# Optimization experiments

Measured on AMD Instinct MI355X. Metric: run time of the kernel, lower is better.

## Reference

```python
import jax, jax.numpy as jnp
import numpy as np

NUM_GRAPHS = 256  # B: number of graphs in the ragged batch
EMBED = 256       # input_dim / MHA embed_dim
N_NODES = 200000


def setup_inputs() -> dict:
    key = jax.random.key(0)
    k1, k2, k3, k4, k5, k6 = jax.random.split(key, 6)
    x = jax.random.normal(k1, (N_NODES, EMBED), dtype=jnp.float32)
    in_proj_w = jax.random.normal(k2, (3 * EMBED, EMBED), dtype=jnp.float32) * 0.02
    in_proj_b = jax.random.normal(k3, (3 * EMBED,), dtype=jnp.float32) * 0.02
    out_proj_w = jax.random.normal(k4, (EMBED, EMBED), dtype=jnp.float32) * 0.02
    out_proj_b = jax.random.normal(k5, (EMBED,), dtype=jnp.float32) * 0.02
    batch = jnp.sort(jax.random.randint(k6, (N_NODES,), 0, NUM_GRAPHS)).astype(jnp.int64)
    return {"x": x, "in_proj_w": in_proj_w, "in_proj_b": in_proj_b,
            "out_proj_w": out_proj_w, "out_proj_b": out_proj_b, "batch": batch}


def reference(x, in_proj_w, in_proj_b, out_proj_w, out_proj_b, batch):
    E = x.shape[1]
    # global_mean_pool: per-graph mean of node features -> [B, E]
    sums = jax.ops.segment_sum(x, batch, num_segments=NUM_GRAPHS)
    counts = jax.ops.segment_sum(jnp.ones((x.shape[0],), x.dtype), batch,
                                 num_segments=NUM_GRAPHS)
    g = sums / jnp.maximum(counts, 1.0)[:, None]  # [B, E]
    # MultiheadAttention with a single K/V vector per graph: softmax over S=1
    # is identically 1, so attention output = out_proj(V_proj(g)) for every
    # query node of that graph (Q path contributes nothing).
    Wv = in_proj_w[2 * E:3 * E]
    bv = in_proj_b[2 * E:3 * E]
    v = g @ Wv.T + bv                       # [B, E] value projection
    out_graph = v @ out_proj_w.T + out_proj_b  # [B, E] output projection
    # broadcast back to nodes (torch.cat over per-graph slices)
    return out_graph[batch]                 # [N, E]
```

## Files before the change

### kernel.cpp

```cpp
#include <hip/hip_runtime.h>

#define EMBED   256
#define NGRAPH  256
#define P       4
#define BLOCK1  512
#define NW1     (BLOCK1 / 64)
#define WPG     (P * NW1)
#define BLOCK3  256
#define NB3     2048

typedef float f32x4 __attribute__((ext_vector_type(4)));

__global__ __launch_bounds__(BLOCK1, 8) void seg_partial(
    const float* __restrict__ x, const int* __restrict__ batch,
    float* __restrict__ partial, int nNodes) {
  const int g  = blockIdx.x >> 2;
  const int p  = blockIdx.x & (P - 1);
  const int t  = threadIdx.x;
  const int q  = t >> 6;
  const int c4 = t & 63;

  int n0, n1;
  { int a = 0, b = nNodes;
    while (a < b) { int m = (a + b) >> 1; (batch[m] < g) ? (a = m + 1) : (b = m); }
    n0 = a; }
  { int a = n0, b = nNodes;
    while (a < b) { int m = (a + b) >> 1; (batch[m] <= g) ? (a = m + 1) : (b = m); }
    n1 = a; }
  const int cnt = n1 - n0;

  const float4* xp = (const float4*)x + (size_t)n0 * (EMBED / 4) + c4;
  const int w = p * NW1 + q;
  float4 a0 = make_float4(0.f, 0.f, 0.f, 0.f);
  float4 a1 = make_float4(0.f, 0.f, 0.f, 0.f);
  int i = w;
  for (; i + 7 * WPG < cnt; i += 8 * WPG) {
    float4 v0 = xp[(size_t)(i          ) * (EMBED / 4)];
    float4 v1 = xp[(size_t)(i + 1 * WPG) * (EMBED / 4)];
    float4 v2 = xp[(size_t)(i + 2 * WPG) * (EMBED / 4)];
    float4 v3 = xp[(size_t)(i + 3 * WPG) * (EMBED / 4)];
    float4 v4 = xp[(size_t)(i + 4 * WPG) * (EMBED / 4)];
    float4 v5 = xp[(size_t)(i + 5 * WPG) * (EMBED / 4)];
    float4 v6 = xp[(size_t)(i + 6 * WPG) * (EMBED / 4)];
    float4 v7 = xp[(size_t)(i + 7 * WPG) * (EMBED / 4)];
    a0.x += v0.x + v1.x; a0.y += v0.y + v1.y; a0.z += v0.z + v1.z; a0.w += v0.w + v1.w;
    a1.x += v2.x + v3.x; a1.y += v2.y + v3.y; a1.z += v2.z + v3.z; a1.w += v2.w + v3.w;
    a0.x += v4.x + v5.x; a0.y += v4.y + v5.y; a0.z += v4.z + v5.z; a0.w += v4.w + v5.w;
    a1.x += v6.x + v7.x; a1.y += v6.y + v7.y; a1.z += v6.z + v7.z; a1.w += v6.w + v7.w;
  }
  for (; i < cnt; i += WPG) {
    float4 v = xp[(size_t)i * (EMBED / 4)];
    a0.x += v.x; a0.y += v.y; a0.z += v.z; a0.w += v.w;
  }
  a0.x += a1.x; a0.y += a1.y; a0.z += a1.z; a0.w += a1.w;

  __shared__ float4 red4[NW1][EMBED / 4];
  red4[q][c4] = a0;
  __syncthreads();
  if (t < EMBED) {
    const float* rf = (const float*)red4;
    float s = 0.f;
#pragma unroll
    for (int k = 0; k < NW1; ++k) s += rf[k * EMBED + t];
    partial[((size_t)p * NGRAPH + g) * EMBED + t] = s;
  }
}

__global__ __launch_bounds__(EMBED, 1) void graph_rows(
    const float* __restrict__ partial, const int* __restrict__ batch,
    const float* __restrict__ in_w, const float* __restrict__ in_b,
    const float* __restrict__ out_w, const float* __restrict__ out_b,
    float* __restrict__ rows, int nNodes) {
  const int g = blockIdx.x;
  const int t = threadIdx.x;

  int n0, n1;
  { int a = 0, b = nNodes;
    while (a < b) { int m = (a + b) >> 1; (batch[m] < g) ? (a = m + 1) : (b = m); }
    n0 = a; }
  { int a = n0, b = nNodes;
    while (a < b) { int m = (a + b) >> 1; (batch[m] <= g) ? (a = m + 1) : (b = m); }
    n1 = a; }
  const float inv = 1.0f / fmaxf((float)(n1 - n0), 1.0f);

  __shared__ float sg[EMBED];
  __shared__ float sv[EMBED];

  float s = 0.f;
#pragma unroll
  for (int p = 0; p < P; ++p) s += partial[((size_t)p * NGRAPH + g) * EMBED + t];
  sg[t] = s * inv;
  __syncthreads();

  float acc = in_b[2 * EMBED + t];
  const float4* wrow = (const float4*)(in_w + (size_t)(2 * EMBED + t) * EMBED);
#pragma unroll 8
  for (int k4 = 0; k4 < EMBED / 4; ++k4) {
    const float4 w = wrow[k4];
    const int k = k4 * 4;
    acc += sg[k] * w.x + sg[k + 1] * w.y + sg[k + 2] * w.z + sg[k + 3] * w.w;
  }
  sv[t] = acc;
  __syncthreads();

  float acc2 = out_b[t];
  const float4* wrow2 = (const float4*)(out_w + (size_t)t * EMBED);
#pragma unroll 8
  for (int k4 = 0; k4 < EMBED / 4; ++k4) {
    const float4 w = wrow2[k4];
    const int k = k4 * 4;
    acc2 += sv[k] * w.x + sv[k + 1] * w.y + sv[k + 2] * w.z + sv[k + 3] * w.w;
  }
  rows[(size_t)g * EMBED + t] = acc2;
}

__global__ __launch_bounds__(BLOCK3, 8) void bcast(
    const float4* __restrict__ rows4, const int* __restrict__ batch,
    float4* __restrict__ out4, long long total) {
  const long long stride = (long long)gridDim.x * BLOCK3;
  long long i = (long long)blockIdx.x * BLOCK3 + threadIdx.x;
  for (; i + 3 * stride < total; i += 4 * stride) {
    const long long i0 = i, i1 = i + stride, i2 = i + 2 * stride, i3 = i + 3 * stride;
    const int g0 = batch[(int)(i0 >> 6)];
    const int g1 = batch[(int)(i1 >> 6)];
    const int g2 = batch[(int)(i2 >> 6)];
    const int g3 = batch[(int)(i3 >> 6)];
    const float4 r0 = rows4[(g0 << 6) + (int)(i0 & 63)];
    const float4 r1 = rows4[(g1 << 6) + (int)(i1 & 63)];
    const float4 r2 = rows4[(g2 << 6) + (int)(i2 & 63)];
    const float4 r3 = rows4[(g3 << 6) + (int)(i3 & 63)];
    __builtin_nontemporal_store(*(const f32x4*)&r0, (f32x4*)(out4 + i0));
    __builtin_nontemporal_store(*(const f32x4*)&r1, (f32x4*)(out4 + i1));
    __builtin_nontemporal_store(*(const f32x4*)&r2, (f32x4*)(out4 + i2));
    __builtin_nontemporal_store(*(const f32x4*)&r3, (f32x4*)(out4 + i3));
  }
  for (; i < total; i += stride) {
    const int gg = batch[(int)(i >> 6)];
    const float4 r = rows4[(gg << 6) + (int)(i & 63)];
    __builtin_nontemporal_store(*(const f32x4*)&r, (f32x4*)(out4 + i));
  }
}

extern "C" void kernel_launch(void* const* d_in, const int* in_sizes, int n_in,
                              void* d_out, int out_size, void* d_ws, size_t ws_size,
                              hipStream_t stream) {
  const float* x     = (const float*)d_in[0];
  const float* in_w  = (const float*)d_in[1];
  const float* in_b  = (const float*)d_in[2];
  const float* out_w = (const float*)d_in[3];
  const float* out_b = (const float*)d_in[4];
  const int*   batch = (const int*)d_in[5];
  const int nNodes = in_sizes[5];

  const size_t needR = (size_t)NGRAPH * EMBED * sizeof(float);
  const size_t needP = (size_t)P * NGRAPH * EMBED * sizeof(float);

  float* rows = (float*)d_ws;
  float* partial;
  if (ws_size >= needR + needP) {
    partial = rows + (size_t)NGRAPH * EMBED;
  } else {
    partial = (float*)d_out;
  }

  seg_partial<<<NGRAPH * P, BLOCK1, 0, stream>>>(x, batch, partial, nNodes);
  graph_rows<<<NGRAPH, EMBED, 0, stream>>>(partial, batch, in_w, in_b,
                                           out_w, out_b, rows, nNodes);
  const long long total = (long long)nNodes * (EMBED / 4);
  bcast<<<NB3, BLOCK3, 0, stream>>>((const float4*)rows, batch,
                                    (float4*)d_out, total);
}
```

Baseline: 386.7 us.

## Fuse segment pooling, projections and broadcast into one kernel with per-graph counters

Replaces the three-kernel pipeline with a single fused kernel. Eight blocks per graph each write a partial sum and bump an atomic counter. The first block of each graph spin-waits for the partials, runs both projections, and publishes the result row. All eight blocks then wait for that row and write the graph's output rows directly, so the separate broadcast pass and its per-element batch lookups go away. This removes kernel launch boundaries and overlaps the broadcast writes with other graphs' reductions. The cost is inter-block spin-waiting, which can deadlock if all blocks are not co-resident, plus an extra init kernel.

```diff
diff --git a/kernel.cpp b/kernel.cpp
--- a/kernel.cpp
+++ b/kernel.cpp
@@ -2,39 +2,53 @@
 
 #define EMBED   256
 #define NGRAPH  256
+
+#define PB      8
+#define TBLOCK  256
+#define NWB     (TBLOCK / 64)
+#define WPG     (PB * NWB)
+
 #define P       4
 #define BLOCK1  512
 #define NW1     (BLOCK1 / 64)
-#define WPG     (P * NW1)
+#define WPG1    (P * NW1)
 #define BLOCK3  256
 #define NB3     2048
 
-typedef float f32x4 __attribute__((ext_vector_type(4)));
-
-__global__ __launch_bounds__(BLOCK1, 8) void seg_partial(
+__device__ __forceinline__ void find_range(const int* __restrict__ batch,
+                                           int nNodes, int g, int& n0, int& n1) {
+  int a = 0, b = nNodes;
+  while (a < b) { int m = (a + b) >> 1; (batch[m] < g) ? (a = m + 1) : (b = m); }
+  n0 = a;
+  b = nNodes;
+  while (a < b) { int m = (a + b) >> 1; (batch[m] <= g) ? (a = m + 1) : (b = m); }
+  n1 = a;
+}
+
+__global__ void init_cnt(int* __restrict__ cnt) { cnt[threadIdx.x] = 0; }
+
+__global__ __launch_bounds__(TBLOCK, 8) void fused_all(
     const float* __restrict__ x, const int* __restrict__ batch,
-    float* __restrict__ partial, int nNodes) {
-  const int g  = blockIdx.x >> 2;
-  const int p  = blockIdx.x & (P - 1);
+    const float* __restrict__ in_w, const float* __restrict__ in_b,
+    const float* __restrict__ out_w, const float* __restrict__ out_b,
+    float* __restrict__ out, int* __restrict__ cnt,
+    float* __restrict__ rows, float* __restrict__ partial, int nNodes) {
+  const int g  = blockIdx.x >> 3;
+  const int p  = blockIdx.x & (PB - 1);
   const int t  = threadIdx.x;
   const int q  = t >> 6;
   const int c4 = t & 63;
 
   int n0, n1;
-  { int a = 0, b = nNodes;
-    while (a < b) { int m = (a + b) >> 1; (batch[m] < g) ? (a = m + 1) : (b = m); }
-    n0 = a; }
-  { int a = n0, b = nNodes;
-    while (a < b) { int m = (a + b) >> 1; (batch[m] <= g) ? (a = m + 1) : (b = m); }
-    n1 = a; }
-  const int cnt = n1 - n0;
+  find_range(batch, nNodes, g, n0, n1);
+  const int cn = n1 - n0;
 
   const float4* xp = (const float4*)x + (size_t)n0 * (EMBED / 4) + c4;
-  const int w = p * NW1 + q;
+  const int w = p * NWB + q;
   float4 a0 = make_float4(0.f, 0.f, 0.f, 0.f);
   float4 a1 = make_float4(0.f, 0.f, 0.f, 0.f);
   int i = w;
-  for (; i + 7 * WPG < cnt; i += 8 * WPG) {
+  for (; i + 7 * WPG < cn; i += 8 * WPG) {
     float4 v0 = xp[(size_t)(i          ) * (EMBED / 4)];
     float4 v1 = xp[(size_t)(i + 1 * WPG) * (EMBED / 4)];
     float4 v2 = xp[(size_t)(i + 2 * WPG) * (EMBED / 4)];
@@ -48,12 +62,105 @@
     a0.x += v4.x + v5.x; a0.y += v4.y + v5.y; a0.z += v4.z + v5.z; a0.w += v4.w + v5.w;
     a1.x += v6.x + v7.x; a1.y += v6.y + v7.y; a1.z += v6.z + v7.z; a1.w += v6.w + v7.w;
   }
-  for (; i < cnt; i += WPG) {
+  for (; i < cn; i += WPG) {
     float4 v = xp[(size_t)i * (EMBED / 4)];
     a0.x += v.x; a0.y += v.y; a0.z += v.z; a0.w += v.w;
   }
   a0.x += a1.x; a0.y += a1.y; a0.z += a1.z; a0.w += a1.w;
 
+  __shared__ float4 red4[NWB][EMBED / 4];
+  __shared__ float sg[EMBED];
+  __shared__ float sv[EMBED];
+  red4[q][c4] = a0;
+  __syncthreads();
+  {
+    const float* rf = (const float*)red4;
+    float s = 0.f;
+#pragma unroll
+    for (int k = 0; k < NWB; ++k) s += rf[k * EMBED + t];
+    partial[((size_t)p * NGRAPH + g) * EMBED + t] = s;
+  }
+  __threadfence();
+  __syncthreads();
+  if (t == 0)
+    __hip_atomic_fetch_add(&cnt[g], 1, __ATOMIC_ACQ_REL, __HIP_MEMORY_SCOPE_AGENT);
+
+  if (p == 0) {
+    if (t == 0)
+      while (__hip_atomic_load(&cnt[g], __ATOMIC_ACQUIRE, __HIP_MEMORY_SCOPE_AGENT) < PB)
+        __builtin_amdgcn_s_sleep(8);
+    __syncthreads();
+
+    const float inv = 1.0f / fmaxf((float)cn, 1.0f);
+    float s = 0.f;
+#pragma unroll
+    for (int pp = 0; pp < PB; ++pp)
+      s += partial[((size_t)pp * NGRAPH + g) * EMBED + t];
+    sg[t] = s * inv;
+    __syncthreads();
+
+    float acc = in_b[2 * EMBED + t];
+    const float4* wrow = (const float4*)(in_w + (size_t)(2 * EMBED + t) * EMBED);
+#pragma unroll 8
+    for (int k4 = 0; k4 < EMBED / 4; ++k4) {
+      const float4 wv = wrow[k4];
+      const int k = k4 * 4;
+      acc += sg[k] * wv.x + sg[k + 1] * wv.y + sg[k + 2] * wv.z + sg[k + 3] * wv.w;
+    }
+    sv[t] = acc;
+    __syncthreads();
+
+    float acc2 = out_b[t];
+    const float4* wrow2 = (const float4*)(out_w + (size_t)t * EMBED);
+#pragma unroll 8
+    for (int k4 = 0; k4 < EMBED / 4; ++k4) {
+      const float4 wv = wrow2[k4];
+      const int k = k4 * 4;
+      acc2 += sv[k] * wv.x + sv[k + 1] * wv.y + sv[k + 2] * wv.z + sv[k + 3] * wv.w;
+    }
+    rows[(size_t)g * EMBED + t] = acc2;
+    __threadfence();
+    __syncthreads();
+    if (t == 0)
+      __hip_atomic_fetch_add(&cnt[g], 1, __ATOMIC_ACQ_REL, __HIP_MEMORY_SCOPE_AGENT);
+  } else {
+    if (t == 0)
+      while (__hip_atomic_load(&cnt[g], __ATOMIC_ACQUIRE, __HIP_MEMORY_SCOPE_AGENT) < PB + 1)
+        __builtin_amdgcn_s_sleep(8);
+    __syncthreads();
+  }
+
+  const float4 oval = ((const float4*)(rows + (size_t)g * EMBED))[c4];
+  float4* op = (float4*)out + c4;
+  int n = n0 + w;
+  for (; n + 3 * WPG < n1; n += 4 * WPG) {
+    op[(size_t)(n          ) * (EMBED / 4)] = oval;
+    op[(size_t)(n + 1 * WPG) * (EMBED / 4)] = oval;
+    op[(size_t)(n + 2 * WPG) * (EMBED / 4)] = oval;
+    op[(size_t)(n + 3 * WPG) * (EMBED / 4)] = oval;
+  }
+  for (; n < n1; n += WPG) op[(size_t)n * (EMBED / 4)] = oval;
+}
+
+__global__ __launch_bounds__(BLOCK1, 8) void seg_partial(
+    const float* __restrict__ x, const int* __restrict__ batch,
+    float* __restrict__ partial, int nNodes) {
+  const int g  = blockIdx.x >> 2;
+  const int p  = blockIdx.x & (P - 1);
+  const int t  = threadIdx.x;
+  const int q  = t >> 6;
+  const int c4 = t & 63;
+  int n0, n1;
+  find_range(batch, nNodes, g, n0, n1);
+  const int cn = n1 - n0;
+  const float4* xp = (const float4*)x + (size_t)n0 * (EMBED / 4) + c4;
+  const int w = p * NW1 + q;
+  float4 a0 = make_float4(0.f, 0.f, 0.f, 0.f);
+  int i = w;
+  for (; i < cn; i += WPG1) {
+    float4 v = xp[(size_t)i * (EMBED / 4)];
+    a0.x += v.x; a0.y += v.y; a0.z += v.z; a0.w += v.w;
+  }
   __shared__ float4 red4[NW1][EMBED / 4];
   red4[q][c4] = a0;
   __syncthreads();
@@ -73,43 +180,33 @@
     float* __restrict__ rows, int nNodes) {
   const int g = blockIdx.x;
   const int t = threadIdx.x;
-
   int n0, n1;
-  { int a = 0, b = nNodes;
-    while (a < b) { int m = (a + b) >> 1; (batch[m] < g) ? (a = m + 1) : (b = m); }
-    n0 = a; }
-  { int a = n0, b = nNodes;
-    while (a < b) { int m = (a + b) >> 1; (batch[m] <= g) ? (a = m + 1) : (b = m); }
-    n1 = a; }
+  find_range(batch, nNodes, g, n0, n1);
   const float inv = 1.0f / fmaxf((float)(n1 - n0), 1.0f);
-
   __shared__ float sg[EMBED];
   __shared__ float sv[EMBED];
-
   float s = 0.f;
 #pragma unroll
-  for (int p = 0; p < P; ++p) s += partial[((size_t)p * NGRAPH + g) * EMBED + t];
+  for (int pp = 0; pp < P; ++pp) s += partial[((size_t)pp * NGRAPH + g) * EMBED + t];
   sg[t] = s * inv;
   __syncthreads();
-
   float acc = in_b[2 * EMBED + t];
   const float4* wrow = (const float4*)(in_w + (size_t)(2 * EMBED + t) * EMBED);
 #pragma unroll 8
   for (int k4 = 0; k4 < EMBED / 4; ++k4) {
-    const float4 w = wrow[k4];
+    const float4 wv = wrow[k4];
     const int k = k4 * 4;
-    acc += sg[k] * w.x + sg[k + 1] * w.y + sg[k + 2] * w.z + sg[k + 3] * w.w;
+    acc += sg[k] * wv.x + sg[k + 1] * wv.y + sg[k + 2] * wv.z + sg[k + 3] * wv.w;
   }
   sv[t] = acc;
   __syncthreads();
-
   float acc2 = out_b[t];
   const float4* wrow2 = (const float4*)(out_w + (size_t)t * EMBED);
 #pragma unroll 8
   for (int k4 = 0; k4 < EMBED / 4; ++k4) {
-    const float4 w = wrow2[k4];
+    const float4 wv = wrow2[k4];
     const int k = k4 * 4;
-    acc2 += sv[k] * w.x + sv[k + 1] * w.y + sv[k + 2] * w.z + sv[k + 3] * w.w;
+    acc2 += sv[k] * wv.x + sv[k + 1] * wv.y + sv[k + 2] * wv.z + sv[k + 3] * wv.w;
   }
   rows[(size_t)g * EMBED + t] = acc2;
 }
@@ -119,25 +216,9 @@
     float4* __restrict__ out4, long long total) {
   const long long stride = (long long)gridDim.x * BLOCK3;
   long long i = (long long)blockIdx.x * BLOCK3 + threadIdx.x;
-  for (; i + 3 * stride < total; i += 4 * stride) {
-    const long long i0 = i, i1 = i + stride, i2 = i + 2 * stride, i3 = i + 3 * stride;
-    const int g0 = batch[(int)(i0 >> 6)];
-    const int g1 = batch[(int)(i1 >> 6)];
-    const int g2 = batch[(int)(i2 >> 6)];
-    const int g3 = batch[(int)(i3 >> 6)];
-    const float4 r0 = rows4[(g0 << 6) + (int)(i0 & 63)];
-    const float4 r1 = rows4[(g1 << 6) + (int)(i1 & 63)];
-    const float4 r2 = rows4[(g2 << 6) + (int)(i2 & 63)];
-    const float4 r3 = rows4[(g3 << 6) + (int)(i3 & 63)];
-    __builtin_nontemporal_store(*(const f32x4*)&r0, (f32x4*)(out4 + i0));
-    __builtin_nontemporal_store(*(const f32x4*)&r1, (f32x4*)(out4 + i1));
-    __builtin_nontemporal_store(*(const f32x4*)&r2, (f32x4*)(out4 + i2));
-    __builtin_nontemporal_store(*(const f32x4*)&r3, (f32x4*)(out4 + i3));
-  }
   for (; i < total; i += stride) {
     const int gg = batch[(int)(i >> 6)];
-    const float4 r = rows4[(gg << 6) + (int)(i & 63)];
-    __builtin_nontemporal_store(*(const f32x4*)&r, (f32x4*)(out4 + i));
+    out4[i] = rows4[(gg << 6) + (int)(i & 63)];
   }
 }
 
@@ -152,17 +233,26 @@
   const int*   batch = (const int*)d_in[5];
   const int nNodes = in_sizes[5];
 
+  const size_t fCnt  = NGRAPH;
+  const size_t fRows = (size_t)NGRAPH * EMBED;
+  const size_t fPart = (size_t)PB * NGRAPH * EMBED;
+  const size_t needFused = (fCnt + fRows + fPart) * sizeof(float);
+
+  if (ws_size >= needFused) {
+    int*   cnt     = (int*)d_ws;
+    float* rows    = (float*)d_ws + fCnt;
+    float* partial = rows + fRows;
+    init_cnt<<<1, NGRAPH, 0, stream>>>(cnt);
+    fused_all<<<NGRAPH * PB, TBLOCK, 0, stream>>>(
+        x, batch, in_w, in_b, out_w, out_b, (float*)d_out, cnt, rows, partial, nNodes);
+    return;
+  }
+
   const size_t needR = (size_t)NGRAPH * EMBED * sizeof(float);
   const size_t needP = (size_t)P * NGRAPH * EMBED * sizeof(float);
-
   float* rows = (float*)d_ws;
-  float* partial;
-  if (ws_size >= needR + needP) {
-    partial = rows + (size_t)NGRAPH * EMBED;
-  } else {
-    partial = (float*)d_out;
-  }
-
+  float* partial = (ws_size >= needR + needP) ? rows + (size_t)NGRAPH * EMBED
+                                              : (float*)d_out;
   seg_partial<<<NGRAPH * P, BLOCK1, 0, stream>>>(x, batch, partial, nNodes);
   graph_rows<<<NGRAPH, EMBED, 0, stream>>>(partial, batch, in_w, in_b,
                                            out_w, out_b, rows, nNodes);
```

New measurement: 1.227 ms. 3.17x slower.
